# Kernel optimization log

Measured on AMD Instinct MI355X. Metric: run time of the kernel, lower is better.

The kernel has to match this reference:

```python
import jax, jax.numpy as jnp
import numpy as np

T = 262144
S_IN, A_IN, S_OUT, G_OUT, H = 64, 16, 32, 16, 32


def setup_inputs() -> dict:
    key = jax.random.key(0)
    ks = jax.random.split(key, 16)
    def lin_w(k, i, o):
        return (jax.random.normal(k, (i, o), jnp.float32) / np.sqrt(i)).astype(jnp.float32)
    return {
        's': jax.random.normal(ks[0], (1, T, S_IN), jnp.float32),
        'a': jax.random.uniform(ks[1], (1, T, A_IN), jnp.float32),  # BCE targets in [0,1]
        'u': jax.random.uniform(ks[2], (1, T, 1), jnp.float32),     # Bernoulli noise
        'W1': lin_w(ks[3], 2 * (S_IN + A_IN), H), 'b1': jnp.zeros((H,), jnp.float32),
        'W2': lin_w(ks[4], 2 * H, H),             'b2': jnp.zeros((H,), jnp.float32),
        'W3': lin_w(ks[5], 2 * H, S_OUT + G_OUT + 1), 'b3': jnp.zeros((S_OUT + G_OUT + 1,), jnp.float32),
        'Wp1': lin_w(ks[6], S_IN + G_OUT, H),     'bp1': jnp.zeros((H,), jnp.float32),
        'Wp2': lin_w(ks[7], H, A_IN),             'bp2': jnp.zeros((A_IN,), jnp.float32),
    }


def gnn_layer(x, W, b):
    # GraphNetLayer: each node sees its own feature + global mean over the trajectory
    agg = jnp.broadcast_to(jnp.mean(x, axis=1, keepdims=True), x.shape)
    return jnp.concatenate([x, agg], axis=-1) @ W + b


def reference(s, a, u, W1, b1, W2, b2, W3, b3, Wp1, bp1, Wp2, bp2):
    # encode: GNN over [N,T,s_in+a_in]
    x = jnp.concatenate([s, a], axis=-1)
    h = jnp.tanh(gnn_layer(x, W1, b1))
    h = jnp.tanh(gnn_layer(h, W2, b2))
    out = gnn_layer(h, W3, b3)
    z, g, alpha_logit = jnp.split(out, [S_OUT, S_OUT + G_OUT], axis=-1)
    alpha = jax.nn.sigmoid(alpha_logit)

    # Bernoulli sample with externalized noise; no gradient through the sample
    hard_alpha = jax.lax.stop_gradient((u < alpha).astype(alpha.dtype))  # [1,T,1]
    log_probs = hard_alpha * jax.nn.log_sigmoid(alpha_logit) + (1.0 - hard_alpha) * jax.nn.log_sigmoid(-alpha_logit)
    reinforce_lp = jnp.mean(log_probs)

    # extend_goals_hard: carry last goal where alpha fired (N==1), ragged scan
    def step(prev, ga):
        gt, at = ga  # [G_OUT], [1]
        cur = jnp.where(at > 0, gt, prev)
        return cur, cur
    _, hard_g = jax.lax.scan(step, jnp.zeros((G_OUT,), g.dtype), (g[0], hard_alpha[0]))
    hard_g = hard_g[None]  # [1,T,G_OUT]

    # decode: goal-conditioned policy MLP
    logits = jnp.tanh(jnp.concatenate([s, hard_g], axis=-1) @ Wp1 + bp1) @ Wp2 + bp2

    # BCEWithLogits recon loss (use_prior=False, train_dynamics/correspondence=False)
    recon = -(a * jax.nn.log_sigmoid(logits) + (1.0 - a) * jax.nn.log_sigmoid(-logits))
    per_ts = recon
    loss = jnp.mean(per_ts) + reinforce_lp * jnp.mean(jax.lax.stop_gradient(per_ts))

    # padded equivalents of short_z/short_g (ragged gather z[0,mask]) returned as masked tensors
    return loss, logits, hard_alpha, hard_g
```

## Files before the change

### kernel.cpp

```cpp
#include <hip/hip_runtime.h>
#include <math.h>


#define TT 262144
#define NBT 1024
#define NBR 512
#define MARGIN 2e-3f
#define LCAP 16384

__device__ __forceinline__ float spf32(float x) {
  return fmaxf(x, 0.f) + log1pf(expf(-fabsf(x)));
}

__device__ __forceinline__ double exp64(double x) {
  const double LOG2E  = 1.4426950408889634074;
  const double LN2_HI = 6.93147180369123816490e-01;
  const double LN2_LO = 1.90821492927058770002e-10;
  double kd = rint(x * LOG2E);
  double r  = fma(-kd, LN2_HI, x);
  r = fma(-kd, LN2_LO, r);
  double p = 2.08767569878681e-9;
  p = fma(p, r, 2.505210838544172e-8);
  p = fma(p, r, 2.755731922398589e-7);
  p = fma(p, r, 2.7557319223985893e-6);
  p = fma(p, r, 2.48015873015873e-5);
  p = fma(p, r, 1.984126984126984e-4);
  p = fma(p, r, 1.388888888888889e-3);
  p = fma(p, r, 8.333333333333333e-3);
  p = fma(p, r, 4.1666666666666664e-2);
  p = fma(p, r, 1.6666666666666666e-1);
  p = fma(p, r, 0.5);
  p = fma(p, r, 1.0);
  p = fma(p, r, 1.0);
  int k = (int)kd;
  long long sb = ((long long)(k + 1023)) << 52;
  return p * __longlong_as_double(sb);
}

__device__ __forceinline__ double tanh64(double x) {
  double ax = fmin(fabs(x), 19.0);
  double e = exp64(2.0 * ax);
  double t = 1.0 - 2.0 / (e + 1.0);
  return x >= 0.0 ? t : -t;
}

template <int C>
__global__ __launch_bounds__(256) void reduce_cols(const float* __restrict__ in,
                                                   double* __restrict__ part) {
  const int rpb = 256 / C;
  int col = threadIdx.x & (C - 1);
  int sub = threadIdx.x / C;
  long row0 = (long)blockIdx.x * rpb + sub;
  long stride = (long)NBR * rpb;
  double acc = 0.0;
  for (long r = row0; r < TT; r += stride) acc += (double)in[r * C + col];
  __shared__ double sm[256];
  sm[threadIdx.x] = acc;
  __syncthreads();
  if (threadIdx.x < C) {
    double s = 0.0;
#pragma unroll
    for (int i = 0; i < rpb; ++i) s += sm[i * C + threadIdx.x];
    part[(long)blockIdx.x * C + threadIdx.x] = s;
  }
}

__global__ __launch_bounds__(640) void prep1(const double* __restrict__ ps_s,
                                             const double* __restrict__ ps_a,
                                             const float* __restrict__ W1,
                                             const float* __restrict__ b1,
                                             double invT, double* __restrict__ c1) {
  __shared__ double partial[80][8];
  __shared__ double mx[80];
  int tid = threadIdx.x;
  int col = tid >> 3, sub = tid & 7;
  double ssum = 0.0;
  if (col < 64) {
#pragma unroll
    for (int i = 0; i < 64; ++i) ssum += ps_s[(sub * 64 + i) * 64 + col];
  } else {
    int c = col - 64;
#pragma unroll
    for (int i = 0; i < 64; ++i) ssum += ps_a[(sub * 64 + i) * 16 + c];
  }
  partial[col][sub] = ssum;
  __syncthreads();
  if (tid < 80) {
    double s = 0.0;
#pragma unroll
    for (int i = 0; i < 8; ++i) s += partial[tid][i];
    mx[tid] = s * invT;
  }
  __syncthreads();
  if (tid < 32) {
    double acc = (double)b1[tid];
    for (int j = 0; j < 80; ++j) acc += mx[j] * (double)W1[(80 + j) * 32 + tid];
    c1[tid] = acc;
  }
}

__global__ __launch_bounds__(256) void prep2(const double* __restrict__ ps,
                                             const float* __restrict__ W2,
                                             const float* __restrict__ b2,
                                             double invT, double* __restrict__ c2) {
  __shared__ double partial[32][8];
  __shared__ double mh[32];
  int tid = threadIdx.x;
  int col = tid >> 3, sub = tid & 7;
  double ssum = 0.0;
#pragma unroll
  for (int i = 0; i < 128; ++i) ssum += ps[(sub * 128 + i) * 32 + col];
  partial[col][sub] = ssum;
  __syncthreads();
  if (tid < 32) {
    double s = 0.0;
#pragma unroll
    for (int i = 0; i < 8; ++i) s += partial[tid][i];
    mh[tid] = s * invT;
  }
  __syncthreads();
  if (tid < 32) {
    double acc = (double)b2[tid];
    for (int j = 0; j < 32; ++j) acc += mh[j] * (double)W2[(32 + j) * 32 + tid];
    c2[tid] = acc;
  }
}

__global__ __launch_bounds__(256) void prep3(const double* __restrict__ ps,
                                             const float* __restrict__ W3,
                                             const float* __restrict__ b3,
                                             double invT, double* __restrict__ c3) {
  __shared__ double partial[32][8];
  __shared__ double mh[32];
  int tid = threadIdx.x;
  int col = tid >> 3, sub = tid & 7;
  double ssum = 0.0;
#pragma unroll
  for (int i = 0; i < 128; ++i) ssum += ps[(sub * 128 + i) * 32 + col];
  partial[col][sub] = ssum;
  __syncthreads();
  if (tid < 32) {
    double s = 0.0;
#pragma unroll
    for (int i = 0; i < 8; ++i) s += partial[tid][i];
    mh[tid] = s * invT;
  }
  __syncthreads();
  if (tid < 17) {
    double acc = (double)b3[32 + tid];
    for (int j = 0; j < 32; ++j) acc += mh[j] * (double)W3[(32 + j) * 49 + 32 + tid];
    c3[tid] = acc;
  }
}


__global__ __launch_bounds__(256, 4) void h1f(const float* __restrict__ s,
                                              const float* __restrict__ a,
                                              const float* __restrict__ W1,
                                              const double* __restrict__ c1,
                                              float* __restrict__ h,
                                              double* __restrict__ ps_h) {
  __shared__ float Wl[80 * 32];
  __shared__ double ws[4 * 32];
  for (int i = threadIdx.x; i < 80 * 32; i += 256) Wl[i] = W1[i];
  __syncthreads();
  long t = (long)blockIdx.x * 256 + threadIdx.x;
  float acc[32];
#pragma unroll
  for (int k = 0; k < 32; ++k) acc[k] = (float)c1[k];
  const float4* s4 = (const float4*)(s + t * 64);
#pragma unroll 2
  for (int q = 0; q < 16; ++q) {
    float4 v = s4[q];
    const float* w = &Wl[(q * 4) * 32];
#pragma unroll
    for (int k = 0; k < 32; ++k)
      acc[k] += v.x * w[k] + v.y * w[32 + k] + v.z * w[64 + k] + v.w * w[96 + k];
  }
  const float4* a4 = (const float4*)(a + t * 16);
#pragma unroll 2
  for (int q = 0; q < 4; ++q) {
    float4 v = a4[q];
    const float* w = &Wl[(64 + q * 4) * 32];
#pragma unroll
    for (int k = 0; k < 32; ++k)
      acc[k] += v.x * w[k] + v.y * w[32 + k] + v.z * w[64 + k] + v.w * w[96 + k];
  }
  float* o = h + (size_t)blockIdx.x * 8192 + threadIdx.x;
#pragma unroll
  for (int k = 0; k < 32; ++k) { acc[k] = tanhf(acc[k]); o[k * 256] = acc[k]; }
  int lane = threadIdx.x & 63, wave = threadIdx.x >> 6;
#pragma unroll
  for (int k = 0; k < 32; ++k) {
    double v = (double)acc[k];
    v += __shfl_down(v, 32, 64); v += __shfl_down(v, 16, 64);
    v += __shfl_down(v, 8, 64);  v += __shfl_down(v, 4, 64);
    v += __shfl_down(v, 2, 64);  v += __shfl_down(v, 1, 64);
    if (lane == 0) ws[wave * 32 + k] = v;
  }
  __syncthreads();
  if (threadIdx.x < 32) {
    double ssum = ws[threadIdx.x] + ws[32 + threadIdx.x] + ws[64 + threadIdx.x] +
                  ws[96 + threadIdx.x];
    ps_h[blockIdx.x * 32 + threadIdx.x] = ssum;
  }
}

__global__ __launch_bounds__(256, 4) void h2f(const float* __restrict__ hin,
                                              const float* __restrict__ W2,
                                              const double* __restrict__ c2,
                                              float* __restrict__ hout,
                                              double* __restrict__ ps_h) {
  __shared__ float Wl[32 * 32];
  __shared__ double ws[4 * 32];
  for (int i = threadIdx.x; i < 32 * 32; i += 256) Wl[i] = W2[i];
  __syncthreads();
  const float* x = hin + (size_t)blockIdx.x * 8192 + threadIdx.x;
  float acc[32];
#pragma unroll
  for (int k = 0; k < 32; ++k) acc[k] = (float)c2[k];
#pragma unroll 4
  for (int j = 0; j < 32; ++j) {
    float xj = x[j * 256];
#pragma unroll
    for (int k = 0; k < 32; ++k) acc[k] += xj * Wl[j * 32 + k];
  }
  float* o = hout + (size_t)blockIdx.x * 8192 + threadIdx.x;
#pragma unroll
  for (int k = 0; k < 32; ++k) { acc[k] = tanhf(acc[k]); o[k * 256] = acc[k]; }
  int lane = threadIdx.x & 63, wave = threadIdx.x >> 6;
#pragma unroll
  for (int k = 0; k < 32; ++k) {
    double v = (double)acc[k];
    v += __shfl_down(v, 32, 64); v += __shfl_down(v, 16, 64);
    v += __shfl_down(v, 8, 64);  v += __shfl_down(v, 4, 64);
    v += __shfl_down(v, 2, 64);  v += __shfl_down(v, 1, 64);
    if (lane == 0) ws[wave * 32 + k] = v;
  }
  __syncthreads();
  if (threadIdx.x < 32) {
    double ssum = ws[threadIdx.x] + ws[32 + threadIdx.x] + ws[64 + threadIdx.x] +
                  ws[96 + threadIdx.x];
    ps_h[blockIdx.x * 32 + threadIdx.x] = ssum;
  }
}

__global__ __launch_bounds__(256, 4) void outf(const float* __restrict__ h,
                                               const float* __restrict__ W3,
                                               const double* __restrict__ c3,
                                               const float* __restrict__ u,
                                               float* __restrict__ g,
                                               float* __restrict__ lvals,
                                               float* __restrict__ ha,
                                               int* __restrict__ cnt,
                                               int* __restrict__ list) {
  __shared__ float Wl[32 * 17];
  for (int i = threadIdx.x; i < 32 * 17; i += 256) {
    int j = i / 17, k = i - j * 17;
    Wl[i] = W3[j * 49 + 32 + k];
  }
  __syncthreads();
  long t = (long)blockIdx.x * 256 + threadIdx.x;
  const float* x = h + (size_t)blockIdx.x * 8192 + threadIdx.x;
  float acc[17];
#pragma unroll
  for (int k = 0; k < 17; ++k) acc[k] = (float)c3[k];
#pragma unroll 4
  for (int j = 0; j < 32; ++j) {
    float xj = x[j * 256];
#pragma unroll
    for (int k = 0; k < 17; ++k) acc[k] += xj * Wl[j * 17 + k];
  }
  float4* g4 = (float4*)(g + t * 16);
  float4 o0, o1, o2, o3;
  o0.x = acc[0];  o0.y = acc[1];  o0.z = acc[2];  o0.w = acc[3];
  o1.x = acc[4];  o1.y = acc[5];  o1.z = acc[6];  o1.w = acc[7];
  o2.x = acc[8];  o2.y = acc[9];  o2.z = acc[10]; o2.w = acc[11];
  o3.x = acc[12]; o3.y = acc[13]; o3.z = acc[14]; o3.w = acc[15];
  g4[0] = o0; g4[1] = o1; g4[2] = o2; g4[3] = o3;
  float l = acc[16];
  lvals[t] = l;
  float uu = u[t];
  float lu = (uu <= 0.f) ? -1e30f : (logf(uu) - logf(1.f - uu));
  float d = l - lu;
  ha[t] = (d > 0.f) ? 1.f : 0.f;
  if (fabsf(d) < MARGIN) {
    int i = atomicAdd(cnt, 1);
    if (i < LCAP) list[i] = (int)t;
  }
}

__global__ __launch_bounds__(256, 4) void fixk(const float* __restrict__ s,
                                               const float* __restrict__ a,
                                               const float* __restrict__ u,
                                               const float* __restrict__ W1,
                                               const float* __restrict__ W2,
                                               const float* __restrict__ W3,
                                               const double* __restrict__ c1,
                                               const double* __restrict__ c2,
                                               const double* __restrict__ c3,
                                               const int* __restrict__ cnt,
                                               const int* __restrict__ list,
                                               float* __restrict__ ha) {
  int n = *cnt;
  if (n > LCAP) n = LCAP;
  int lane = threadIdx.x & 63;
  int wid = (blockIdx.x * 256 + threadIdx.x) >> 6;
  const int nw = (64 * 256) >> 6;
  int col = lane & 31;
  for (int i = wid; i < n; i += nw) {
    int row = list[i];
    double acc = c1[col];
    for (int j = 0; j < 64; ++j)
      acc += (double)s[(size_t)row * 64 + j] * (double)W1[j * 32 + col];
    for (int j = 0; j < 16; ++j)
      acc += (double)a[(size_t)row * 16 + j] * (double)W1[(64 + j) * 32 + col];
    double h1v = tanh64(acc);
    double acc2 = c2[col];
    for (int j = 0; j < 32; ++j)
      acc2 += __shfl(h1v, j, 64) * (double)W2[j * 32 + col];
    double h2v = tanh64(acc2);
    double term = h2v * (double)W3[col * 49 + 48];
    term += __shfl_down(term, 16, 64);
    term += __shfl_down(term, 8, 64);
    term += __shfl_down(term, 4, 64);
    term += __shfl_down(term, 2, 64);
    term += __shfl_down(term, 1, 64);
    if (lane == 0) {
      double l = c3[16] + term;
      double lc = fmin(fmax(l, -700.0), 700.0);
      double alpha = 1.0 / (1.0 + exp64(-lc));
      ha[row] = (((double)u[row]) < alpha) ? 1.f : 0.f;
    }
  }
}

__global__ __launch_bounds__(256, 4) void statsk(const float* __restrict__ ha,
                                                 const float* __restrict__ lvals,
                                                 int* __restrict__ lastf,
                                                 double* __restrict__ lp_part) {
  __shared__ double sm[256];
  __shared__ unsigned long long wm[4];
  long t = (long)blockIdx.x * 256 + threadIdx.x;
  bool fired = ha[t] > 0.5f;
  float lf = lvals[t];
  sm[threadIdx.x] = (double)(fired ? -spf32(-lf) : -spf32(lf));
  unsigned long long bm = __ballot(fired ? 1 : 0);
  if ((threadIdx.x & 63) == 0) wm[threadIdx.x >> 6] = bm;
  __syncthreads();
  for (int off = 128; off > 0; off >>= 1) {
    if (threadIdx.x < off) sm[threadIdx.x] += sm[threadIdx.x + off];
    __syncthreads();
  }
  if (threadIdx.x == 0) {
    lp_part[blockIdx.x] = sm[0];
    int last = -1;
#pragma unroll
    for (int w = 3; w >= 0; --w) {
      if (last < 0 && wm[w])
        last = (int)((long)blockIdx.x * 256 + w * 64 + (63 - __builtin_clzll(wm[w])));
    }
    lastf[blockIdx.x] = last;
  }
}

__global__ __launch_bounds__(1024) void carry_scan(const int* __restrict__ lastf,
                                                   int* __restrict__ carry, int n) {
  __shared__ int sm[1024];
  int tid = threadIdx.x;
  sm[tid] = (tid < n) ? lastf[tid] : -1;
  __syncthreads();
  for (int off = 1; off < n; off <<= 1) {
    int v = sm[tid];
    int o = (tid >= off) ? sm[tid - off] : -1;
    __syncthreads();
    sm[tid] = v > o ? v : o;
    __syncthreads();
  }
  if (tid < n) carry[tid] = (tid == 0) ? -1 : sm[tid - 1];
}

__global__ __launch_bounds__(256, 2) void decode_kernel(
    const float* __restrict__ s, const float* __restrict__ a, const float* __restrict__ g,
    const float* __restrict__ Wp1, const float* __restrict__ bp1, const float* __restrict__ Wp2,
    const float* __restrict__ bp2, const float* __restrict__ ha, const int* __restrict__ carry,
    float* __restrict__ logits, float* __restrict__ hardg, double* __restrict__ rc_part) {
  __shared__ float W1l[80 * 32];
  __shared__ float W2l[32 * 16];
  __shared__ int wlast[4];
  __shared__ double sm[256];
  long t = (long)blockIdx.x * 256 + threadIdx.x;
  bool fired = ha[t] > 0.5f;
  unsigned long long m = __ballot(fired ? 1 : 0);
  int wave = threadIdx.x >> 6, lane = threadIdx.x & 63;
  if (lane == 0)
    wlast[wave] = m ? (int)((long)blockIdx.x * 256 + wave * 64 + (63 - __builtin_clzll(m))) : -1;
  for (int i = threadIdx.x; i < 80 * 32; i += 256) W1l[i] = Wp1[i];
  for (int i = threadIdx.x; i < 32 * 16; i += 256) W2l[i] = Wp2[i];
  __syncthreads();
  unsigned long long pm = m & (~0ULL >> (63 - lane));
  int idx = pm ? (int)((long)blockIdx.x * 256 + wave * 64 + (63 - __builtin_clzll(pm))) : -1;
#pragma unroll
  for (int w = 0; w < 4; ++w)
    if (w < wave && wlast[w] > idx) idx = wlast[w];
  int cr = carry[blockIdx.x];
  if (cr > idx) idx = cr;
  float msk = idx >= 0 ? 1.f : 0.f;
  const float4* g4 = (const float4*)(g + (long)(idx >= 0 ? idx : 0) * 16);
  float4 v0 = g4[0], v1 = g4[1], v2 = g4[2], v3 = g4[3];
  float hg0  = msk * v0.x, hg1  = msk * v0.y, hg2  = msk * v0.z, hg3  = msk * v0.w;
  float hg4  = msk * v1.x, hg5  = msk * v1.y, hg6  = msk * v1.z, hg7  = msk * v1.w;
  float hg8  = msk * v2.x, hg9  = msk * v2.y, hg10 = msk * v2.z, hg11 = msk * v2.w;
  float hg12 = msk * v3.x, hg13 = msk * v3.y, hg14 = msk * v3.z, hg15 = msk * v3.w;
  hardg[t * 16 + 0]  = hg0;  hardg[t * 16 + 1]  = hg1;
  hardg[t * 16 + 2]  = hg2;  hardg[t * 16 + 3]  = hg3;
  hardg[t * 16 + 4]  = hg4;  hardg[t * 16 + 5]  = hg5;
  hardg[t * 16 + 6]  = hg6;  hardg[t * 16 + 7]  = hg7;
  hardg[t * 16 + 8]  = hg8;  hardg[t * 16 + 9]  = hg9;
  hardg[t * 16 + 10] = hg10; hardg[t * 16 + 11] = hg11;
  hardg[t * 16 + 12] = hg12; hardg[t * 16 + 13] = hg13;
  hardg[t * 16 + 14] = hg14; hardg[t * 16 + 15] = hg15;
  float acc[32];
#pragma unroll
  for (int k = 0; k < 32; ++k) {
    float v = bp1[k];
    v += hg0  * W1l[(64 + 0)  * 32 + k];  v += hg1  * W1l[(64 + 1)  * 32 + k];
    v += hg2  * W1l[(64 + 2)  * 32 + k];  v += hg3  * W1l[(64 + 3)  * 32 + k];
    v += hg4  * W1l[(64 + 4)  * 32 + k];  v += hg5  * W1l[(64 + 5)  * 32 + k];
    v += hg6  * W1l[(64 + 6)  * 32 + k];  v += hg7  * W1l[(64 + 7)  * 32 + k];
    v += hg8  * W1l[(64 + 8)  * 32 + k];  v += hg9  * W1l[(64 + 9)  * 32 + k];
    v += hg10 * W1l[(64 + 10) * 32 + k];  v += hg11 * W1l[(64 + 11) * 32 + k];
    v += hg12 * W1l[(64 + 12) * 32 + k];  v += hg13 * W1l[(64 + 13) * 32 + k];
    v += hg14 * W1l[(64 + 14) * 32 + k];  v += hg15 * W1l[(64 + 15) * 32 + k];
    acc[k] = v;
  }
  const float4* s4 = (const float4*)(s + t * 64);
#pragma unroll 4
  for (int q = 0; q < 16; ++q) {
    float4 v = s4[q];
    const float* w = &W1l[(q * 4) * 32];
#pragma unroll
    for (int k = 0; k < 32; ++k)
      acc[k] += v.x * w[k] + v.y * w[32 + k] + v.z * w[64 + k] + v.w * w[96 + k];
  }
#pragma unroll
  for (int k = 0; k < 32; ++k) acc[k] = tanhf(acc[k]);
  float lg[16];
#pragma unroll
  for (int k = 0; k < 16; ++k) lg[k] = bp2[k];
#pragma unroll
  for (int j = 0; j < 32; ++j) {
    float hj = acc[j];
    const float* w = &W2l[j * 16];
#pragma unroll
    for (int k = 0; k < 16; ++k) lg[k] += hj * w[k];
  }
#pragma unroll
  for (int k = 0; k < 16; ++k) logits[t * 16 + k] = lg[k];
  const float4* a4 = (const float4*)(a + t * 16);
  double rs = 0.0;
#pragma unroll
  for (int q = 0; q < 4; ++q) {
    float4 av = a4[q];
    float l0 = lg[q * 4], l1 = lg[q * 4 + 1], l2 = lg[q * 4 + 2], l3 = lg[q * 4 + 3];
    rs += (double)(av.x * spf32(-l0) + (1.f - av.x) * spf32(l0));
    rs += (double)(av.y * spf32(-l1) + (1.f - av.y) * spf32(l1));
    rs += (double)(av.z * spf32(-l2) + (1.f - av.z) * spf32(l2));
    rs += (double)(av.w * spf32(-l3) + (1.f - av.w) * spf32(l3));
  }
  sm[threadIdx.x] = rs;
  __syncthreads();
  for (int off = 128; off > 0; off >>= 1) {
    if (threadIdx.x < off) sm[threadIdx.x] += sm[threadIdx.x + off];
    __syncthreads();
  }
  if (threadIdx.x == 0) rc_part[blockIdx.x] = sm[0];
}

__global__ __launch_bounds__(256) void finalize(const double* __restrict__ lp_part,
                                                const double* __restrict__ rc_part, int nb,
                                                double invT, float* __restrict__ out0) {
  __shared__ double s1[256], s2[256];
  int tid = threadIdx.x;
  double a1 = 0, a2 = 0;
  for (int i = tid; i < nb; i += 256) { a1 += lp_part[i]; a2 += rc_part[i]; }
  s1[tid] = a1; s2[tid] = a2;
  __syncthreads();
  for (int off = 128; off > 0; off >>= 1) {
    if (tid < off) { s1[tid] += s1[tid + off]; s2[tid] += s2[tid + off]; }
    __syncthreads();
  }
  if (tid == 0) {
    double R = s1[0] * invT;
    double M = s2[0] * invT / 16.0;
    out0[0] = (float)(M + R * M);
  }
}

extern "C" void kernel_launch(void* const* d_in, const int* in_sizes, int n_in,
                              void* d_out, int out_size, void* d_ws, size_t ws_size,
                              hipStream_t stream) {
  const float* s   = (const float*)d_in[0];
  const float* a   = (const float*)d_in[1];
  const float* u   = (const float*)d_in[2];
  const float* W1  = (const float*)d_in[3];
  const float* b1  = (const float*)d_in[4];
  const float* W2  = (const float*)d_in[5];
  const float* b2  = (const float*)d_in[6];
  const float* W3  = (const float*)d_in[7];
  const float* b3  = (const float*)d_in[8];
  const float* Wp1 = (const float*)d_in[9];
  const float* bp1 = (const float*)d_in[10];
  const float* Wp2 = (const float*)d_in[11];
  const float* bp2 = (const float*)d_in[12];

  const double invT = 1.0 / (double)TT;

  double* ps_s   = (double*)d_ws;
  double* ps_a   = ps_s + (size_t)NBR * 64;
  double* ps_h   = ps_a + (size_t)NBR * 16;
  double* c1     = ps_h + (size_t)NBT * 32;
  double* c2     = c1 + 32;
  double* c3     = c2 + 32;
  double* lp     = c3 + 24;
  double* rc     = lp + NBT;
  float*  g      = (float*)(rc + NBT);
  float*  h      = g + (size_t)TT * 16;
  float*  lvals  = h + (size_t)TT * 32;
  int*    lastf  = (int*)(lvals + TT);
  int*    carry  = lastf + NBT;
  int*    cnt    = carry + NBT;
  int*    list   = cnt + 4;

  float* out    = (float*)d_out;
  float* loss   = out;
  float* logits = out + 1;
  float* ha     = out + 1 + (size_t)TT * 16;
  float* hg     = ha + TT;

  hipMemsetAsync((void*)cnt, 0, sizeof(int), stream);
  reduce_cols<64><<<NBR, 256, 0, stream>>>(s, ps_s);
  reduce_cols<16><<<NBR, 256, 0, stream>>>(a, ps_a);
  prep1<<<1, 640, 0, stream>>>(ps_s, ps_a, W1, b1, invT, c1);
  h1f<<<NBT, 256, 0, stream>>>(s, a, W1, c1, h, ps_h);
  prep2<<<1, 256, 0, stream>>>(ps_h, W2, b2, invT, c2);
  h2f<<<NBT, 256, 0, stream>>>(h, W2, c2, h, ps_h);
  prep3<<<1, 256, 0, stream>>>(ps_h, W3, b3, invT, c3);
  outf<<<NBT, 256, 0, stream>>>(h, W3, c3, u, g, lvals, ha, cnt, list);
  fixk<<<64, 256, 0, stream>>>(s, a, u, W1, W2, W3, c1, c2, c3, cnt, list, ha);
  statsk<<<NBT, 256, 0, stream>>>(ha, lvals, lastf, lp);
  carry_scan<<<1, NBT, 0, stream>>>(lastf, carry, NBT);
  decode_kernel<<<NBT, 256, 0, stream>>>(s, a, g, Wp1, bp1, Wp2, bp2, ha, carry,
                                         logits, hg, rc);
  finalize<<<1, 256, 0, stream>>>(lp, rc, NBT, invT, loss);
}
```

Before: 331.1 us.

## Recompute layer-2 activations in output kernel and merge column reductions

```diff
diff --git a/kernel.cpp b/kernel.cpp
--- a/kernel.cpp
+++ b/kernel.cpp
@@ -44,24 +44,42 @@
   return x >= 0.0 ? t : -t;
 }
 
-template <int C>
-__global__ __launch_bounds__(256) void reduce_cols(const float* __restrict__ in,
-                                                   double* __restrict__ part) {
-  const int rpb = 256 / C;
-  int col = threadIdx.x & (C - 1);
-  int sub = threadIdx.x / C;
-  long row0 = (long)blockIdx.x * rpb + sub;
-  long stride = (long)NBR * rpb;
-  double acc = 0.0;
-  for (long r = row0; r < TT; r += stride) acc += (double)in[r * C + col];
+__global__ __launch_bounds__(256) void reduce_sa(const float* __restrict__ s,
+                                                 const float* __restrict__ a,
+                                                 double* __restrict__ ps_s,
+                                                 double* __restrict__ ps_a) {
   __shared__ double sm[256];
-  sm[threadIdx.x] = acc;
-  __syncthreads();
-  if (threadIdx.x < C) {
-    double s = 0.0;
-#pragma unroll
-    for (int i = 0; i < rpb; ++i) s += sm[i * C + threadIdx.x];
-    part[(long)blockIdx.x * C + threadIdx.x] = s;
+  {
+    int col = threadIdx.x & 63;
+    int sub = threadIdx.x >> 6;
+    long row0 = (long)blockIdx.x * 4 + sub;
+    long stride = (long)NBR * 4;
+    double acc = 0.0;
+    for (long r = row0; r < TT; r += stride) acc += (double)s[r * 64 + col];
+    sm[threadIdx.x] = acc;
+    __syncthreads();
+    if (threadIdx.x < 64) {
+      double ss = sm[threadIdx.x] + sm[64 + threadIdx.x] + sm[128 + threadIdx.x] +
+                  sm[192 + threadIdx.x];
+      ps_s[(long)blockIdx.x * 64 + threadIdx.x] = ss;
+    }
+    __syncthreads();
+  }
+  {
+    int col = threadIdx.x & 15;
+    int sub = threadIdx.x >> 4;
+    long row0 = (long)blockIdx.x * 16 + sub;
+    long stride = (long)NBR * 16;
+    double acc = 0.0;
+    for (long r = row0; r < TT; r += stride) acc += (double)a[r * 16 + col];
+    sm[threadIdx.x] = acc;
+    __syncthreads();
+    if (threadIdx.x < 16) {
+      double ss = 0.0;
+#pragma unroll
+      for (int i = 0; i < 16; ++i) ss += sm[i * 16 + threadIdx.x];
+      ps_a[(long)blockIdx.x * 16 + threadIdx.x] = ss;
+    }
   }
 }
 
@@ -153,8 +171,27 @@
   }
 }
 
-
-__global__ __launch_bounds__(256, 4) void h1f(const float* __restrict__ s,
+__device__ __forceinline__ void colsum32_f32(const float* acc, double* ws,
+                                             double* ps_h, int bid) {
+  int lane = threadIdx.x & 63, wave = threadIdx.x >> 6;
+#pragma unroll
+  for (int k = 0; k < 32; ++k) {
+    float v = acc[k];
+    v += __shfl_down(v, 32, 64); v += __shfl_down(v, 16, 64);
+    v += __shfl_down(v, 8, 64);  v += __shfl_down(v, 4, 64);
+    v += __shfl_down(v, 2, 64);  v += __shfl_down(v, 1, 64);
+    if (lane == 0) ws[wave * 32 + k] = (double)v;
+  }
+  __syncthreads();
+  if (threadIdx.x < 32) {
+    double ssum = ws[threadIdx.x] + ws[32 + threadIdx.x] + ws[64 + threadIdx.x] +
+                  ws[96 + threadIdx.x];
+    ps_h[bid * 32 + threadIdx.x] = ssum;
+  }
+}
+
+
+__global__ __launch_bounds__(256, 6) void h1f(const float* __restrict__ s,
                                               const float* __restrict__ a,
                                               const float* __restrict__ W1,
                                               const double* __restrict__ c1,
@@ -189,33 +226,18 @@
   float* o = h + (size_t)blockIdx.x * 8192 + threadIdx.x;
 #pragma unroll
   for (int k = 0; k < 32; ++k) { acc[k] = tanhf(acc[k]); o[k * 256] = acc[k]; }
-  int lane = threadIdx.x & 63, wave = threadIdx.x >> 6;
-#pragma unroll
-  for (int k = 0; k < 32; ++k) {
-    double v = (double)acc[k];
-    v += __shfl_down(v, 32, 64); v += __shfl_down(v, 16, 64);
-    v += __shfl_down(v, 8, 64);  v += __shfl_down(v, 4, 64);
-    v += __shfl_down(v, 2, 64);  v += __shfl_down(v, 1, 64);
-    if (lane == 0) ws[wave * 32 + k] = v;
-  }
-  __syncthreads();
-  if (threadIdx.x < 32) {
-    double ssum = ws[threadIdx.x] + ws[32 + threadIdx.x] + ws[64 + threadIdx.x] +
-                  ws[96 + threadIdx.x];
-    ps_h[blockIdx.x * 32 + threadIdx.x] = ssum;
-  }
-}
-
-__global__ __launch_bounds__(256, 4) void h2f(const float* __restrict__ hin,
-                                              const float* __restrict__ W2,
-                                              const double* __restrict__ c2,
-                                              float* __restrict__ hout,
-                                              double* __restrict__ ps_h) {
+  colsum32_f32(acc, ws, ps_h, blockIdx.x);
+}
+
+__global__ __launch_bounds__(256, 6) void h2cs(const float* __restrict__ h1,
+                                               const float* __restrict__ W2,
+                                               const double* __restrict__ c2,
+                                               double* __restrict__ ps_h) {
   __shared__ float Wl[32 * 32];
   __shared__ double ws[4 * 32];
   for (int i = threadIdx.x; i < 32 * 32; i += 256) Wl[i] = W2[i];
   __syncthreads();
-  const float* x = hin + (size_t)blockIdx.x * 8192 + threadIdx.x;
+  const float* x = h1 + (size_t)blockIdx.x * 8192 + threadIdx.x;
   float acc[32];
 #pragma unroll
   for (int k = 0; k < 32; ++k) acc[k] = (float)c2[k];
@@ -225,27 +247,14 @@
 #pragma unroll
     for (int k = 0; k < 32; ++k) acc[k] += xj * Wl[j * 32 + k];
   }
-  float* o = hout + (size_t)blockIdx.x * 8192 + threadIdx.x;
-#pragma unroll
-  for (int k = 0; k < 32; ++k) { acc[k] = tanhf(acc[k]); o[k * 256] = acc[k]; }
-  int lane = threadIdx.x & 63, wave = threadIdx.x >> 6;
-#pragma unroll
-  for (int k = 0; k < 32; ++k) {
-    double v = (double)acc[k];
-    v += __shfl_down(v, 32, 64); v += __shfl_down(v, 16, 64);
-    v += __shfl_down(v, 8, 64);  v += __shfl_down(v, 4, 64);
-    v += __shfl_down(v, 2, 64);  v += __shfl_down(v, 1, 64);
-    if (lane == 0) ws[wave * 32 + k] = v;
-  }
-  __syncthreads();
-  if (threadIdx.x < 32) {
-    double ssum = ws[threadIdx.x] + ws[32 + threadIdx.x] + ws[64 + threadIdx.x] +
-                  ws[96 + threadIdx.x];
-    ps_h[blockIdx.x * 32 + threadIdx.x] = ssum;
-  }
-}
-
-__global__ __launch_bounds__(256, 4) void outf(const float* __restrict__ h,
+#pragma unroll
+  for (int k = 0; k < 32; ++k) acc[k] = tanhf(acc[k]);
+  colsum32_f32(acc, ws, ps_h, blockIdx.x);
+}
+
+__global__ __launch_bounds__(256, 6) void outf(const float* __restrict__ h1,
+                                               const float* __restrict__ W2,
+                                               const double* __restrict__ c2,
                                                const float* __restrict__ W3,
                                                const double* __restrict__ c3,
                                                const float* __restrict__ u,
@@ -254,22 +263,35 @@
                                                float* __restrict__ ha,
                                                int* __restrict__ cnt,
                                                int* __restrict__ list) {
-  __shared__ float Wl[32 * 17];
+  __shared__ float W2l[32 * 32];
+  __shared__ float W3l[32 * 17];
+  for (int i = threadIdx.x; i < 32 * 32; i += 256) W2l[i] = W2[i];
   for (int i = threadIdx.x; i < 32 * 17; i += 256) {
     int j = i / 17, k = i - j * 17;
-    Wl[i] = W3[j * 49 + 32 + k];
+    W3l[i] = W3[j * 49 + 32 + k];
   }
   __syncthreads();
   long t = (long)blockIdx.x * 256 + threadIdx.x;
-  const float* x = h + (size_t)blockIdx.x * 8192 + threadIdx.x;
-  float acc[17];
-#pragma unroll
-  for (int k = 0; k < 17; ++k) acc[k] = (float)c3[k];
+  const float* x = h1 + (size_t)blockIdx.x * 8192 + threadIdx.x;
+  float h2r[32];
+#pragma unroll
+  for (int k = 0; k < 32; ++k) h2r[k] = (float)c2[k];
 #pragma unroll 4
   for (int j = 0; j < 32; ++j) {
     float xj = x[j * 256];
 #pragma unroll
-    for (int k = 0; k < 17; ++k) acc[k] += xj * Wl[j * 17 + k];
+    for (int k = 0; k < 32; ++k) h2r[k] += xj * W2l[j * 32 + k];
+  }
+#pragma unroll
+  for (int k = 0; k < 32; ++k) h2r[k] = tanhf(h2r[k]);
+  float acc[17];
+#pragma unroll
+  for (int k = 0; k < 17; ++k) acc[k] = (float)c3[k];
+#pragma unroll
+  for (int j = 0; j < 32; ++j) {
+    float xj = h2r[j];
+#pragma unroll
+    for (int k = 0; k < 17; ++k) acc[k] += xj * W3l[j * 17 + k];
   }
   float4* g4 = (float4*)(g + t * 16);
   float4 o0, o1, o2, o3;
@@ -380,7 +402,7 @@
   if (tid < n) carry[tid] = (tid == 0) ? -1 : sm[tid - 1];
 }
 
-__global__ __launch_bounds__(256, 2) void decode_kernel(
+__global__ __launch_bounds__(256, 3) void decode_kernel(
     const float* __restrict__ s, const float* __restrict__ a, const float* __restrict__ g,
     const float* __restrict__ Wp1, const float* __restrict__ bp1, const float* __restrict__ Wp2,
     const float* __restrict__ bp2, const float* __restrict__ ha, const int* __restrict__ carry,
@@ -539,14 +561,13 @@
   float* hg     = ha + TT;
 
   hipMemsetAsync((void*)cnt, 0, sizeof(int), stream);
-  reduce_cols<64><<<NBR, 256, 0, stream>>>(s, ps_s);
-  reduce_cols<16><<<NBR, 256, 0, stream>>>(a, ps_a);
+  reduce_sa<<<NBR, 256, 0, stream>>>(s, a, ps_s, ps_a);
   prep1<<<1, 640, 0, stream>>>(ps_s, ps_a, W1, b1, invT, c1);
   h1f<<<NBT, 256, 0, stream>>>(s, a, W1, c1, h, ps_h);
   prep2<<<1, 256, 0, stream>>>(ps_h, W2, b2, invT, c2);
-  h2f<<<NBT, 256, 0, stream>>>(h, W2, c2, h, ps_h);
+  h2cs<<<NBT, 256, 0, stream>>>(h, W2, c2, ps_h);
   prep3<<<1, 256, 0, stream>>>(ps_h, W3, b3, invT, c3);
-  outf<<<NBT, 256, 0, stream>>>(h, W3, c3, u, g, lvals, ha, cnt, list);
+  outf<<<NBT, 256, 0, stream>>>(h, W2, c2, W3, c3, u, g, lvals, ha, cnt, list);
   fixk<<<64, 256, 0, stream>>>(s, a, u, W1, W2, W3, c1, c2, c3, cnt, list, ha);
   statsk<<<NBT, 256, 0, stream>>>(ha, lvals, lastf, lp);
   carry_scan<<<1, NBT, 0, stream>>>(lastf, carry, NBT);
```

Result: slower. 971.6 us (+193.4%).
